# Kernel optimization log

Measured on AMD Instinct MI355X. Metric: run time of the kernel, lower is better.

The kernel has to match this reference:

```python
import jax, jax.numpy as jnp
import numpy as np

N_NODES = 50000
E_EDGES = 1600000
C_IN = 64
C_OUT = 64
K_CHEB = 3


def _norm(edge_index, edge_weight, n):
    # PyG ChebConv.__norm__ with normalization='sym', lambda_max=2.0:
    # remove self loops, sym-normalized Laplacian scaled by 2/lambda_max, then
    # subtract identity -> L_hat has zero diagonal and off-diag -d^-1/2 w d^-1/2.
    row, col = edge_index[0], edge_index[1]
    mask = row != col
    ew = jnp.where(mask, edge_weight, 0.0)
    deg = jax.ops.segment_sum(ew, row, num_segments=n)  # [N]
    dinv = jnp.where(deg > 0, jax.lax.rsqrt(jnp.where(deg > 0, deg, 1.0)), 0.0)
    wn = -ew * dinv[row] * dinv[col]  # [E], zero on (removed) self loops
    return row, col, wn


def _propagate(x, row, col, wn, n):
    # y = L_hat @ x via edge gather + weighted scatter-add
    return jax.ops.segment_sum(wn[:, None] * x[col], row, num_segments=n)


def _cheb(x, W, b, row, col, wn, n):
    # Chebyshev recursion: Tx0=x, Tx1=L_hat x, Txk = 2 L_hat Tx(k-1) - Tx(k-2)
    out = x @ W[0]
    Tx0, Tx1 = x, None
    if W.shape[0] > 1:
        Tx1 = _propagate(x, row, col, wn, n)
        out = out + Tx1 @ W[1]
    for k in range(2, W.shape[0]):
        Tx2 = 2.0 * _propagate(Tx1, row, col, wn, n) - Tx0
        out = out + Tx2 @ W[k]
        Tx0, Tx1 = Tx1, Tx2
    return out + b


def setup_inputs() -> dict:
    key = jax.random.key(0)
    ks = jax.random.split(key, 40)
    d = {
        'X': jax.random.normal(ks[0], (N_NODES, C_IN), jnp.float32),
        'edge_index': jax.random.randint(ks[1], (2, E_EDGES), 0, N_NODES),
        'edge_weight': jax.random.uniform(ks[2], (E_EDGES,), jnp.float32),
        'H': jax.random.normal(ks[3], (N_NODES, C_OUT), jnp.float32) * 0.1,
        'C': jax.random.normal(ks[4], (N_NODES, C_OUT), jnp.float32) * 0.1,
    }
    i = 5
    sx = 1.0 / np.sqrt(C_IN)
    sh = 1.0 / np.sqrt(C_OUT)
    for nm in ['xi', 'xf', 'xc', 'xo']:
        d['W_' + nm] = jax.random.normal(ks[i], (K_CHEB, C_IN, C_OUT), jnp.float32) * sx; i += 1
        d['bc_' + nm] = jax.random.normal(ks[i], (C_OUT,), jnp.float32) * 0.02; i += 1
    for nm in ['hi', 'hf', 'hc', 'ho']:
        d['W_' + nm] = jax.random.normal(ks[i], (K_CHEB, C_OUT, C_OUT), jnp.float32) * sh; i += 1
        d['bc_' + nm] = jax.random.normal(ks[i], (C_OUT,), jnp.float32) * 0.02; i += 1
    for nm in ['w_ci', 'w_cf', 'w_co', 'b_i', 'b_f', 'b_c', 'b_o']:
        d[nm] = jax.random.normal(ks[i], (1, C_OUT), jnp.float32) * 0.1; i += 1
    return d


def reference(X, edge_index, edge_weight, H, C,
              W_xi, bc_xi, W_xf, bc_xf, W_xc, bc_xc, W_xo, bc_xo,
              W_hi, bc_hi, W_hf, bc_hf, W_hc, bc_hc, W_ho, bc_ho,
              w_ci, w_cf, w_co, b_i, b_f, b_c, b_o):
    n = X.shape[0]
    row, col, wn = _norm(edge_index, edge_weight, n)
    I = jax.nn.sigmoid(_cheb(X, W_xi, bc_xi, row, col, wn, n)
                       + _cheb(H, W_hi, bc_hi, row, col, wn, n)
                       + w_ci * C + b_i)
    Fg = jax.nn.sigmoid(_cheb(X, W_xf, bc_xf, row, col, wn, n)
                        + _cheb(H, W_hf, bc_hf, row, col, wn, n)
                        + w_cf * C + b_f)
    T = jnp.tanh(_cheb(X, W_xc, bc_xc, row, col, wn, n)
                 + _cheb(H, W_hc, bc_hc, row, col, wn, n)
                 + b_c)
    C_new = Fg * C + I * T
    O = jax.nn.sigmoid(_cheb(X, W_xo, bc_xo, row, col, wn, n)
                       + _cheb(H, W_ho, bc_ho, row, col, wn, n)
                       + w_co * C_new + b_o)
    H_new = O * jnp.tanh(C_new)
    return (H_new, C_new)
```

## Files before the change

### kernel.cpp

```cpp
#include <hip/hip_runtime.h>
#include <hip/hip_bf16.h>
#include <math.h>

#define N_NODES 50000
#define E_EDGES 1600000
#define NBKT 196
#define PBLK 400
#define CHUNK 4000

typedef __attribute__((ext_vector_type(8))) short s8v;
typedef __attribute__((ext_vector_type(4))) float f32x4;

#define O_BLKH  0
#define O_BBASE 78592
#define O_BSUM  78848
#define O_CNT   79104
#define O_DINV  129152
#define O_RPTR  179200
#define O_SREC  229248
#define O_SREC2 3429248
#define O_EDGE  O_SREC
#define O_XHB   O_SREC2
#define O_T1B   6629248
#define O_T2B   9829248
#define O_BP    13029248

__device__ __forceinline__ uint pk_bf16(float x, float y) {
  __hip_bfloat16 bx = __float2bfloat16(x), by = __float2bfloat16(y);
  ushort ux = *reinterpret_cast<ushort*>(&bx);
  ushort uy = *reinterpret_cast<ushort*>(&by);
  return ((uint)uy << 16) | (uint)ux;
}

__global__ __launch_bounds__(256) void k_hist(const int* __restrict__ ei,
                                              uint* __restrict__ blkh) {
  __shared__ uint h[NBKT];
  int blk = blockIdx.x, tid = threadIdx.x;
  for (int i = tid; i < NBKT; i += 256) h[i] = 0;
  __syncthreads();
  int e0 = blk * CHUNK;
  for (int i = tid; i < CHUNK; i += 256) {
    int e = e0 + i;
    int r = ei[e], c = ei[E_EDGES + e];
    if (r != c) atomicAdd(&h[r >> 8], 1u);
  }
  __syncthreads();
  for (int i = tid; i < NBKT; i += 256) blkh[i * PBLK + blk] = h[i];
}

__global__ __launch_bounds__(256) void k_bsum_scan(uint* __restrict__ blkh,
                                                   uint* __restrict__ bsum) {
  __shared__ uint sh[512];
  int b = blockIdx.x, t = threadIdx.x;
  uint v0 = (t < PBLK) ? blkh[b * PBLK + t] : 0u;
  uint v1 = (t + 256 < PBLK) ? blkh[b * PBLK + t + 256] : 0u;
  sh[t] = v0; sh[t + 256] = v1;
  __syncthreads();
  for (int off = 1; off < 512; off <<= 1) {
    uint x0 = sh[t], x1 = sh[t + 256];
    uint a0 = (t >= off) ? sh[t - off] : 0u;
    uint a1 = (t + 256 >= off) ? sh[t + 256 - off] : 0u;
    __syncthreads();
    sh[t] = x0 + a0; sh[t + 256] = x1 + a1;
    __syncthreads();
  }
  if (t < PBLK) blkh[b * PBLK + t] = sh[t] - v0;
  if (t + 256 < PBLK) blkh[b * PBLK + t + 256] = sh[t + 256] - v1;
  if (t == 0) bsum[b] = sh[511];
}

__global__ __launch_bounds__(256) void k_bscan(const uint* __restrict__ bsum,
                                               uint* __restrict__ bbase) {
  __shared__ uint sh[256];
  int t = threadIdx.x;
  uint v = (t < NBKT) ? bsum[t] : 0u;
  sh[t] = v;
  __syncthreads();
  for (int off = 1; off < 256; off <<= 1) {
    uint a = (t >= off) ? sh[t - off] : 0u;
    __syncthreads();
    sh[t] += a;
    __syncthreads();
  }
  if (t < NBKT) bbase[t] = sh[t] - v;
  if (t == 255) bbase[NBKT] = sh[255];
}

__global__ __launch_bounds__(256) void k_scatter_b(const int* __restrict__ ei,
                                                   const float* __restrict__ ew,
                                                   const uint* __restrict__ off,
                                                   const uint* __restrict__ bbase,
                                                   unsigned long long* __restrict__ srec) {
  __shared__ uint cur[NBKT];
  int blk = blockIdx.x, tid = threadIdx.x;
  for (int i = tid; i < NBKT; i += 256) cur[i] = off[i * PBLK + blk] + bbase[i];
  __syncthreads();
  int e0 = blk * CHUNK;
  for (int i = tid; i < CHUNK; i += 256) {
    int e = e0 + i;
    int r = ei[e], c = ei[E_EDGES + e];
    if (r != c) {
      uint pos = atomicAdd(&cur[r >> 8], 1u);
      srec[pos] = ((unsigned long long)(r & 255) << 48) |
                  ((unsigned long long)(uint)c << 32) |
                  (unsigned long long)__float_as_uint(ew[e]);
    }
  }
}

__global__ __launch_bounds__(256) void k_csr(const unsigned long long* __restrict__ srec,
                                             const uint* __restrict__ bbase,
                                             unsigned long long* __restrict__ srec2,
                                             int* __restrict__ cnt, float* __restrict__ dinv,
                                             int* __restrict__ rptr) {
  __shared__ uint hc[256], hs[256], cur[256], wsum[4];
  int b = blockIdx.x, t = threadIdx.x;
  uint start = bbase[b], endv = bbase[b + 1];
  hc[t] = 0; hs[t] = 0;
  __syncthreads();
  for (uint i = start + t; i < endv; i += 256) {
    unsigned long long rec = srec[i];
    int rl = (int)(rec >> 48);
    float w = __uint_as_float((uint)rec);
    atomicAdd(&hc[rl], 1u);
    atomicAdd(&hs[rl], (uint)(w * 1048576.0f + 0.5f));
  }
  __syncthreads();
  int lane = t & 63, wid = t >> 6;
  uint myc = hc[t];
  uint x = myc;
#pragma unroll
  for (int off = 1; off < 64; off <<= 1) {
    uint y = __shfl_up(x, off);
    if (lane >= off) x += y;
  }
  if (lane == 63) wsum[wid] = x;
  __syncthreads();
  uint woff = 0;
#pragma unroll
  for (int j = 0; j < 4; ++j) if (j < wid) woff += wsum[j];
  uint excl = woff + x - myc;
  int row = b * 256 + t;
  if (row < N_NODES) {
    float d = (float)hs[t] * (1.0f / 1048576.0f);
    dinv[row] = d > 0.f ? rsqrtf(d) : 0.f;
    cnt[row] = (int)myc;
    rptr[row] = (int)(start + excl);
  }
  cur[t] = start + excl;
  __syncthreads();
  for (uint i = start + t; i < endv; i += 256) {
    unsigned long long rec = srec[i];
    int rl = (int)(rec >> 48);
    uint pos = atomicAdd(&cur[rl], 1u);
    srec2[pos] = rec;
  }
}

__global__ __launch_bounds__(256) void k_finalize(const unsigned long long* __restrict__ srec2,
                                                  const uint* __restrict__ bbase,
                                                  const float* __restrict__ dinv,
                                                  uint* __restrict__ edges) {
  int b = blockIdx.x, t = threadIdx.x;
  uint start = bbase[b], endv = bbase[b + 1];
  for (uint i = start + t; i < endv; i += 256) {
    unsigned long long rec = srec2[i];
    int rl = (int)(rec >> 48);
    int c = (int)((rec >> 32) & 0xffff);
    float w = __uint_as_float((uint)rec);
    int r = b * 256 + rl;
    float wn = -w * dinv[r] * dinv[c];
    __hip_bfloat16 bw = __float2bfloat16(wn);
    edges[i] = ((uint)c << 16) | (uint)*reinterpret_cast<ushort*>(&bw);
  }
}

__global__ void k_xhb(const float* __restrict__ X, const float* __restrict__ Hm,
                      uint* __restrict__ XHb) {
  int t = blockIdx.x * blockDim.x + threadIdx.x;
  if (t >= N_NODES * 64) return;
  int n = t >> 6, q = t & 63;
  float2 v = (q < 32) ? *(const float2*)(X + (long)n * 64 + q * 2)
                      : *(const float2*)(Hm + (long)n * 64 + (q - 32) * 2);
  XHb[t] = pk_bf16(v.x, v.y);
}

__global__ __launch_bounds__(256) void k_spmm2b(
    const uint* __restrict__ src, const uint* __restrict__ other,
    float alpha, float beta,
    const int* __restrict__ rptr, const int* __restrict__ cnt,
    const uint* __restrict__ edges, uint* __restrict__ out) {
  int wid = threadIdx.x >> 6, lane = threadIdx.x & 63;
  int row = blockIdx.x * 4 + wid;
  if (row >= N_NODES) return;
  int start = rptr[row], n = cnt[row];
  int half = lane >> 5;
  int l5 = lane & 31;
  float ax = 0.f, ay = 0.f, bx = 0.f, by = 0.f;
  for (int base = 0; base < n; base += 64) {
    int m = n - base; if (m > 64) m = 64;
    uint rec = (lane < m) ? edges[start + base + lane] : 0u;
    int iters = (m + 1) >> 1;
    int j = 0;
    for (; j + 4 <= iters; j += 4) {
#pragma unroll
      for (int u = 0; u < 4; ++u) {
        uint r = __shfl(rec, 2 * (j + u) + half);
        int cc = (int)(r >> 16);
        float ww = __uint_as_float(r << 16);
        uint2 z = *(const uint2*)(src + cc * 64 + (l5 << 1));
        ax = fmaf(ww, __uint_as_float(z.x << 16), ax);
        ay = fmaf(ww, __uint_as_float(z.x & 0xffff0000u), ay);
        bx = fmaf(ww, __uint_as_float(z.y << 16), bx);
        by = fmaf(ww, __uint_as_float(z.y & 0xffff0000u), by);
      }
    }
    for (; j < iters; ++j) {
      uint r = __shfl(rec, 2 * j + half);
      int cc = (int)(r >> 16);
      float ww = __uint_as_float(r << 16);
      uint2 z = *(const uint2*)(src + cc * 64 + (l5 << 1));
      ax = fmaf(ww, __uint_as_float(z.x << 16), ax);
      ay = fmaf(ww, __uint_as_float(z.x & 0xffff0000u), ay);
      bx = fmaf(ww, __uint_as_float(z.y << 16), bx);
      by = fmaf(ww, __uint_as_float(z.y & 0xffff0000u), by);
    }
  }
  ax += __shfl_xor(ax, 32); ay += __shfl_xor(ay, 32);
  bx += __shfl_xor(bx, 32); by += __shfl_xor(by, 32);
  if (half == 0) {
    long o = (long)row * 64 + (l5 << 1);
    float ox = alpha * ax, oy = alpha * ay;
    float px = alpha * bx, py = alpha * by;
    if (beta != 0.f) {
      uint2 ov = *(const uint2*)(other + o);
      ox += beta * __uint_as_float(ov.x << 16);
      oy += beta * __uint_as_float(ov.x & 0xffff0000u);
      px += beta * __uint_as_float(ov.y << 16);
      py += beta * __uint_as_float(ov.y & 0xffff0000u);
    }
    uint2 w2; w2.x = pk_bf16(ox, oy); w2.y = pk_bf16(px, py);
    *(uint2*)(out + o) = w2;
  }
}

__global__ void k_pack(const float* __restrict__ Wxi, const float* __restrict__ Wxf,
                       const float* __restrict__ Wxc, const float* __restrict__ Wxo,
                       const float* __restrict__ Whi, const float* __restrict__ Whf,
                       const float* __restrict__ Whc, const float* __restrict__ Who,
                       ushort* __restrict__ Bp) {
  int idx = blockIdx.x * blockDim.x + threadIdx.x;
  if (idx >= 12 * 16 * 64 * 8) return;
  int j = idx & 7;
  int lane = (idx >> 3) & 63;
  int c = (idx >> 9) & 15;
  int t = idx >> 13;
  int k = t * 32 + (lane >> 4) * 8 + j;
  int col = c * 16 + (lane & 15);
  int g = col >> 6, oc = col & 63;
  int s = k >> 6, kk = k & 63, ord = s >> 1;
  const float* Wx[4] = {Wxi, Wxf, Wxc, Wxo};
  const float* Wh[4] = {Whi, Whf, Whc, Who};
  const float* W = (s & 1) ? Wh[g] : Wx[g];
  float v = W[(ord * 64 + kk) * 64 + oc];
  __hip_bfloat16 b = __float2bfloat16(v);
  Bp[idx] = *reinterpret_cast<ushort*>(&b);
}

__device__ __forceinline__ float frcp(float x) { return __builtin_amdgcn_rcpf(x); }

__global__ __launch_bounds__(256) void k_mfma_lstm(
    const uint* __restrict__ XHb, const uint* __restrict__ T1b,
    const uint* __restrict__ T2b, const float* __restrict__ C,
    const ushort* __restrict__ Bp,
    const float* __restrict__ bxi, const float* __restrict__ bxf,
    const float* __restrict__ bxc, const float* __restrict__ bxo,
    const float* __restrict__ bhi, const float* __restrict__ bhf,
    const float* __restrict__ bhc, const float* __restrict__ bho,
    const float* __restrict__ wci, const float* __restrict__ wcf, const float* __restrict__ wco,
    const float* __restrict__ bi, const float* __restrict__ bf_,
    const float* __restrict__ bc_, const float* __restrict__ bo,
    float* __restrict__ Hout, float* __restrict__ Cout) {
  int lane = threadIdx.x & 63, wid = threadIdx.x >> 6;
  int row0 = blockIdx.x * 64 + wid * 16;
  int ar = row0 + (lane & 15);
  if (ar > N_NODES - 1) ar = N_NODES - 1;

  const ushort* XHs = (const ushort*)XHb;
  const ushort* T1s = (const ushort*)T1b;
  const ushort* T2s = (const ushort*)T2b;
  long abase = (long)ar * 128 + (lane >> 4) * 8;
  s8v a[12];
#pragma unroll
  for (int q = 0; q < 4; ++q) a[q] = *(const s8v*)(XHs + abase + q * 32);
#pragma unroll
  for (int q = 0; q < 4; ++q) a[4 + q] = *(const s8v*)(T1s + abase + q * 32);
#pragma unroll
  for (int q = 0; q < 4; ++q) a[8 + q] = *(const s8v*)(T2s + abase + q * 32);

  const ushort* bp = Bp + lane * 8;
  f32x4 acc[16];
#pragma unroll
  for (int c = 0; c < 16; ++c) acc[c] = {0.f, 0.f, 0.f, 0.f};

  s8v bA[16], bB[16];
#pragma unroll
  for (int c = 0; c < 16; ++c) bA[c] = *(const s8v*)(bp + c * 512);
#pragma unroll
  for (int t = 0; t < 12; ++t) {
    if (t & 1) {
      if (t < 11) {
#pragma unroll
        for (int c = 0; c < 16; ++c)
          bA[c] = *(const s8v*)(bp + (t + 1) * 8192 + c * 512);
      }
#pragma unroll
      for (int c = 0; c < 16; ++c)
        acc[c] = __builtin_amdgcn_mfma_f32_16x16x32_bf16(a[t], bB[c], acc[c], 0, 0, 0);
    } else {
      if (t < 11) {
#pragma unroll
        for (int c = 0; c < 16; ++c)
          bB[c] = *(const s8v*)(bp + (t + 1) * 8192 + c * 512);
      }
#pragma unroll
      for (int c = 0; c < 16; ++c)
        acc[c] = __builtin_amdgcn_mfma_f32_16x16x32_bf16(a[t], bA[c], acc[c], 0, 0, 0);
    }
  }

  int rbase = row0 + ((lane >> 4) << 2);
  int ocl = lane & 15;
#pragma unroll
  for (int j = 0; j < 4; ++j) {
    int oc = j * 16 + ocl;
    float bI = bxi[oc] + bhi[oc] + bi[oc];
    float bF = bxf[oc] + bhf[oc] + bf_[oc];
    float bT = bxc[oc] + bhc[oc] + bc_[oc];
    float bO = bxo[oc] + bho[oc] + bo[oc];
    float wcI = wci[oc], wcF = wcf[oc], wcO = wco[oc];
#pragma unroll
    for (int r = 0; r < 4; ++r) {
      int row = rbase + r;
      if (row < N_NODES) {
        float cv = C[(long)row * 64 + oc];
        float I = frcp(1.f + __expf(-(acc[j][r] + bI + wcI * cv)));
        float F = frcp(1.f + __expf(-(acc[4 + j][r] + bF + wcF * cv)));
        float e2 = __expf(2.f * (acc[8 + j][r] + bT));
        float T = 1.f - 2.f * frcp(e2 + 1.f);
        float cn = F * cv + I * T;
        float O = frcp(1.f + __expf(-(acc[12 + j][r] + bO + wcO * cn)));
        float e2c = __expf(2.f * cn);
        float tc = 1.f - 2.f * frcp(e2c + 1.f);
        Hout[(long)row * 64 + oc] = O * tc;
        Cout[(long)row * 64 + oc] = cn;
      }
    }
  }
}

extern "C" void kernel_launch(void* const* d_in, const int* in_sizes, int n_in,
                              void* d_out, int out_size, void* d_ws, size_t ws_size,
                              hipStream_t stream) {
  (void)in_sizes; (void)n_in; (void)out_size; (void)ws_size;
  const float* X   = (const float*)d_in[0];
  const int*   ei  = (const int*)d_in[1];
  const float* ew  = (const float*)d_in[2];
  const float* H   = (const float*)d_in[3];
  const float* C   = (const float*)d_in[4];
  const float* Wxi = (const float*)d_in[5];
  const float* bxi = (const float*)d_in[6];
  const float* Wxf = (const float*)d_in[7];
  const float* bxf = (const float*)d_in[8];
  const float* Wxc = (const float*)d_in[9];
  const float* bxc = (const float*)d_in[10];
  const float* Wxo = (const float*)d_in[11];
  const float* bxo = (const float*)d_in[12];
  const float* Whi = (const float*)d_in[13];
  const float* bhi = (const float*)d_in[14];
  const float* Whf = (const float*)d_in[15];
  const float* bhf = (const float*)d_in[16];
  const float* Whc = (const float*)d_in[17];
  const float* bhc = (const float*)d_in[18];
  const float* Who = (const float*)d_in[19];
  const float* bho = (const float*)d_in[20];
  const float* wci = (const float*)d_in[21];
  const float* wcf = (const float*)d_in[22];
  const float* wco = (const float*)d_in[23];
  const float* bi  = (const float*)d_in[24];
  const float* bf_ = (const float*)d_in[25];
  const float* bc_ = (const float*)d_in[26];
  const float* bo  = (const float*)d_in[27];

  float* ws = (float*)d_ws;
  uint*   blkh  = (uint*)(ws + O_BLKH);
  uint*   bbase = (uint*)(ws + O_BBASE);
  uint*   bsum  = (uint*)(ws + O_BSUM);
  int*    cnt   = (int*)(ws + O_CNT);
  float*  dinv  = ws + O_DINV;
  int*    rptr  = (int*)(ws + O_RPTR);
  unsigned long long* srec  = (unsigned long long*)(ws + O_SREC);
  unsigned long long* srec2 = (unsigned long long*)(ws + O_SREC2);
  uint*   edges = (uint*)(ws + O_EDGE);
  uint*   XHb   = (uint*)(ws + O_XHB);
  uint*   T1b   = (uint*)(ws + O_T1B);
  uint*   T2b   = (uint*)(ws + O_T2B);
  ushort* Bp    = (ushort*)(ws + O_BP);

  float* Hout = (float*)d_out;
  float* Cout = Hout + N_NODES * 64;

  k_hist<<<PBLK, 256, 0, stream>>>(ei, blkh);
  k_bsum_scan<<<NBKT, 256, 0, stream>>>(blkh, bsum);
  k_bscan<<<1, 256, 0, stream>>>(bsum, bbase);
  k_scatter_b<<<PBLK, 256, 0, stream>>>(ei, ew, blkh, bbase, srec);
  k_csr<<<NBKT, 256, 0, stream>>>(srec, bbase, srec2, cnt, dinv, rptr);
  k_finalize<<<NBKT, 256, 0, stream>>>(srec2, bbase, dinv, edges);
  k_xhb<<<(N_NODES * 64 + 255) / 256, 256, 0, stream>>>(X, H, XHb);
  k_pack<<<(12 * 16 * 64 * 8 + 255) / 256, 256, 0, stream>>>(Wxi, Wxf, Wxc, Wxo,
                                                             Whi, Whf, Whc, Who, Bp);
  int spmm_grid = (N_NODES + 3) / 4;
  k_spmm2b<<<spmm_grid, 256, 0, stream>>>(XHb, XHb, 1.f, 0.f, rptr, cnt, edges, T1b);
  k_spmm2b<<<spmm_grid, 256, 0, stream>>>(T1b, XHb, 2.f, -1.f, rptr, cnt, edges, T2b);
  k_mfma_lstm<<<(N_NODES + 63) / 64, 256, 0, stream>>>(
      XHb, T1b, T2b, C, Bp,
      bxi, bxf, bxc, bxo, bhi, bhf, bhc, bho,
      wci, wcf, wco, bi, bf_, bc_, bo, Hout, Cout);
}
```

Baseline: 221.4 us.

## Switch fused LSTM GEMM to 32x32x16 MFMA with one-wave blocks

The dense GEMM+LSTM kernel is rewritten around the 32x32x16 bf16 MFMA. Each 64-thread block now covers 32 rows, so every B fragment feeds twice as many rows. The weight packing kernel is changed to match the new fragment layout. A and B fragments are double-buffered across 24 k-steps and the epilogue is remapped to the 32x32 accumulator layout. This aims to cut weight-load traffic per row and MFMA issue count, at the cost of smaller blocks and higher register pressure.

```diff
diff --git a/kernel.cpp b/kernel.cpp
--- a/kernel.cpp
+++ b/kernel.cpp
@@ -9,7 +9,7 @@
 #define CHUNK 4000
 
 typedef __attribute__((ext_vector_type(8))) short s8v;
-typedef __attribute__((ext_vector_type(4))) float f32x4;
+typedef __attribute__((ext_vector_type(16))) float f32x16;
 
 #define O_BLKH  0
 #define O_BBASE 78592
@@ -250,13 +250,13 @@
                        const float* __restrict__ Whc, const float* __restrict__ Who,
                        ushort* __restrict__ Bp) {
   int idx = blockIdx.x * blockDim.x + threadIdx.x;
-  if (idx >= 12 * 16 * 64 * 8) return;
+  if (idx >= 24 * 8 * 64 * 8) return;
   int j = idx & 7;
   int lane = (idx >> 3) & 63;
-  int c = (idx >> 9) & 15;
-  int t = idx >> 13;
-  int k = t * 32 + (lane >> 4) * 8 + j;
-  int col = c * 16 + (lane & 15);
+  int ct = (idx >> 9) & 7;
+  int st = idx >> 12;
+  int k = st * 16 + (lane >> 5) * 8 + j;
+  int col = ct * 32 + (lane & 31);
   int g = col >> 6, oc = col & 63;
   int s = k >> 6, kk = k & 63, ord = s >> 1;
   const float* Wx[4] = {Wxi, Wxf, Wxc, Wxo};
@@ -269,7 +269,7 @@
 
 __device__ __forceinline__ float frcp(float x) { return __builtin_amdgcn_rcpf(x); }
 
-__global__ __launch_bounds__(256) void k_mfma_lstm(
+__global__ __launch_bounds__(64, 2) void k_mfma_lstm(
     const uint* __restrict__ XHb, const uint* __restrict__ T1b,
     const uint* __restrict__ T2b, const float* __restrict__ C,
     const ushort* __restrict__ Bp,
@@ -281,75 +281,63 @@
     const float* __restrict__ bi, const float* __restrict__ bf_,
     const float* __restrict__ bc_, const float* __restrict__ bo,
     float* __restrict__ Hout, float* __restrict__ Cout) {
-  int lane = threadIdx.x & 63, wid = threadIdx.x >> 6;
-  int row0 = blockIdx.x * 64 + wid * 16;
-  int ar = row0 + (lane & 15);
+  int lane = threadIdx.x & 63;
+  int row0 = blockIdx.x * 32;
+  int ar = row0 + (lane & 31);
   if (ar > N_NODES - 1) ar = N_NODES - 1;
 
   const ushort* XHs = (const ushort*)XHb;
   const ushort* T1s = (const ushort*)T1b;
   const ushort* T2s = (const ushort*)T2b;
-  long abase = (long)ar * 128 + (lane >> 4) * 8;
-  s8v a[12];
-#pragma unroll
-  for (int q = 0; q < 4; ++q) a[q] = *(const s8v*)(XHs + abase + q * 32);
-#pragma unroll
-  for (int q = 0; q < 4; ++q) a[4 + q] = *(const s8v*)(T1s + abase + q * 32);
-#pragma unroll
-  for (int q = 0; q < 4; ++q) a[8 + q] = *(const s8v*)(T2s + abase + q * 32);
-
+  long arow = (long)ar * 128 + (lane >> 5) * 8;
   const ushort* bp = Bp + lane * 8;
-  f32x4 acc[16];
-#pragma unroll
-  for (int c = 0; c < 16; ++c) acc[c] = {0.f, 0.f, 0.f, 0.f};
-
-  s8v bA[16], bB[16];
-#pragma unroll
-  for (int c = 0; c < 16; ++c) bA[c] = *(const s8v*)(bp + c * 512);
-#pragma unroll
-  for (int t = 0; t < 12; ++t) {
-    if (t & 1) {
-      if (t < 11) {
-#pragma unroll
-        for (int c = 0; c < 16; ++c)
-          bA[c] = *(const s8v*)(bp + (t + 1) * 8192 + c * 512);
-      }
-#pragma unroll
-      for (int c = 0; c < 16; ++c)
-        acc[c] = __builtin_amdgcn_mfma_f32_16x16x32_bf16(a[t], bB[c], acc[c], 0, 0, 0);
-    } else {
-      if (t < 11) {
-#pragma unroll
-        for (int c = 0; c < 16; ++c)
-          bB[c] = *(const s8v*)(bp + (t + 1) * 8192 + c * 512);
-      }
-#pragma unroll
-      for (int c = 0; c < 16; ++c)
-        acc[c] = __builtin_amdgcn_mfma_f32_16x16x32_bf16(a[t], bA[c], acc[c], 0, 0, 0);
-    }
-  }
-
-  int rbase = row0 + ((lane >> 4) << 2);
-  int ocl = lane & 15;
-#pragma unroll
-  for (int j = 0; j < 4; ++j) {
-    int oc = j * 16 + ocl;
+
+  f32x16 acc[8] = {};
+
+  s8v aC, aN;
+  s8v bC[8], bN[8];
+  aC = *(const s8v*)(XHs + arow);
+#pragma unroll
+  for (int c = 0; c < 8; ++c) bC[c] = *(const s8v*)(bp + c * 512);
+
+#pragma unroll
+  for (int st = 0; st < 24; ++st) {
+    if (st < 23) {
+      const ushort* S = (st + 1 < 8) ? XHs : ((st + 1 < 16) ? T1s : T2s);
+      aN = *(const s8v*)(S + arow + ((st + 1) & 7) * 16);
+#pragma unroll
+      for (int c = 0; c < 8; ++c)
+        bN[c] = *(const s8v*)(bp + ((st + 1) * 8 + c) * 512);
+    }
+#pragma unroll
+    for (int c = 0; c < 8; ++c)
+      acc[c] = __builtin_amdgcn_mfma_f32_32x32x16_bf16(aC, bC[c], acc[c], 0, 0, 0);
+    aC = aN;
+#pragma unroll
+    for (int c = 0; c < 8; ++c) bC[c] = bN[c];
+  }
+
+  int colb = lane & 31;
+  int rsel = 4 * (lane >> 5);
+#pragma unroll
+  for (int half = 0; half < 2; ++half) {
+    int oc = half * 32 + colb;
     float bI = bxi[oc] + bhi[oc] + bi[oc];
     float bF = bxf[oc] + bhf[oc] + bf_[oc];
     float bT = bxc[oc] + bhc[oc] + bc_[oc];
     float bO = bxo[oc] + bho[oc] + bo[oc];
     float wcI = wci[oc], wcF = wcf[oc], wcO = wco[oc];
 #pragma unroll
-    for (int r = 0; r < 4; ++r) {
-      int row = rbase + r;
+    for (int r = 0; r < 16; ++r) {
+      int row = row0 + (r & 3) + 8 * (r >> 2) + rsel;
       if (row < N_NODES) {
         float cv = C[(long)row * 64 + oc];
-        float I = frcp(1.f + __expf(-(acc[j][r] + bI + wcI * cv)));
-        float F = frcp(1.f + __expf(-(acc[4 + j][r] + bF + wcF * cv)));
-        float e2 = __expf(2.f * (acc[8 + j][r] + bT));
+        float I = frcp(1.f + __expf(-(acc[0 + half][r] + bI + wcI * cv)));
+        float F = frcp(1.f + __expf(-(acc[2 + half][r] + bF + wcF * cv)));
+        float e2 = __expf(2.f * (acc[4 + half][r] + bT));
         float T = 1.f - 2.f * frcp(e2 + 1.f);
         float cn = F * cv + I * T;
-        float O = frcp(1.f + __expf(-(acc[12 + j][r] + bO + wcO * cn)));
+        float O = frcp(1.f + __expf(-(acc[6 + half][r] + bO + wcO * cn)));
         float e2c = __expf(2.f * cn);
         float tc = 1.f - 2.f * frcp(e2c + 1.f);
         Hout[(long)row * 64 + oc] = O * tc;
@@ -417,12 +405,12 @@
   k_csr<<<NBKT, 256, 0, stream>>>(srec, bbase, srec2, cnt, dinv, rptr);
   k_finalize<<<NBKT, 256, 0, stream>>>(srec2, bbase, dinv, edges);
   k_xhb<<<(N_NODES * 64 + 255) / 256, 256, 0, stream>>>(X, H, XHb);
-  k_pack<<<(12 * 16 * 64 * 8 + 255) / 256, 256, 0, stream>>>(Wxi, Wxf, Wxc, Wxo,
-                                                             Whi, Whf, Whc, Who, Bp);
+  k_pack<<<(24 * 8 * 64 * 8 + 255) / 256, 256, 0, stream>>>(Wxi, Wxf, Wxc, Wxo,
+                                                            Whi, Whf, Whc, Who, Bp);
   int spmm_grid = (N_NODES + 3) / 4;
   k_spmm2b<<<spmm_grid, 256, 0, stream>>>(XHb, XHb, 1.f, 0.f, rptr, cnt, edges, T1b);
   k_spmm2b<<<spmm_grid, 256, 0, stream>>>(T1b, XHb, 2.f, -1.f, rptr, cnt, edges, T2b);
-  k_mfma_lstm<<<(N_NODES + 63) / 64, 256, 0, stream>>>(
+  k_mfma_lstm<<<(N_NODES + 31) / 32, 64, 0, stream>>>(
       XHb, T1b, T2b, C, Bp,
       bxi, bxf, bxc, bxo, bhi, bhf, bhc, bho,
       wci, wcf, wco, bi, bf_, bc_, bo, Hout, Cout);
```

Measured after the change: 229.6 us. 1.04x slower.

## Split gate columns across waves in LSTM MFMA kernel and vectorize epilogue via LDS

Applied to the files above, without the earlier changes.

The fused gate GEMM kernel now assigns 16 rows per block, with each of the four waves computing one gate's 64 output columns. Previously each wave held 16 rows times all 256 columns, using 16 accumulators, 12 A registers and 32 B registers. The smaller per-wave register footprint should raise occupancy and increase the block count. Gate results go through a shared-memory tile so the LSTM epilogue can work row-wise with float4 loads and stores of C, H and biases. The cost is that the weight matrix B is reloaded per block four times as often, and a barrier is added.

```diff
diff --git a/kernel.cpp b/kernel.cpp
--- a/kernel.cpp
+++ b/kernel.cpp
@@ -281,81 +281,94 @@
     const float* __restrict__ bi, const float* __restrict__ bf_,
     const float* __restrict__ bc_, const float* __restrict__ bo,
     float* __restrict__ Hout, float* __restrict__ Cout) {
-  int lane = threadIdx.x & 63, wid = threadIdx.x >> 6;
-  int row0 = blockIdx.x * 64 + wid * 16;
+  __shared__ float gsh[16][260];
+  int tid = threadIdx.x;
+  int lane = tid & 63, wid = tid >> 6;
+  int row0 = blockIdx.x * 16;
   int ar = row0 + (lane & 15);
-  if (ar > N_NODES - 1) ar = N_NODES - 1;
+  long abase = (long)ar * 128 + (lane >> 4) * 8;
 
   const ushort* XHs = (const ushort*)XHb;
   const ushort* T1s = (const ushort*)T1b;
   const ushort* T2s = (const ushort*)T2b;
-  long abase = (long)ar * 128 + (lane >> 4) * 8;
-  s8v a[12];
-#pragma unroll
-  for (int q = 0; q < 4; ++q) a[q] = *(const s8v*)(XHs + abase + q * 32);
-#pragma unroll
-  for (int q = 0; q < 4; ++q) a[4 + q] = *(const s8v*)(T1s + abase + q * 32);
-#pragma unroll
-  for (int q = 0; q < 4; ++q) a[8 + q] = *(const s8v*)(T2s + abase + q * 32);
-
-  const ushort* bp = Bp + lane * 8;
-  f32x4 acc[16];
-#pragma unroll
-  for (int c = 0; c < 16; ++c) acc[c] = {0.f, 0.f, 0.f, 0.f};
-
-  s8v bA[16], bB[16];
-#pragma unroll
-  for (int c = 0; c < 16; ++c) bA[c] = *(const s8v*)(bp + c * 512);
+  const ushort* bpg = Bp + (long)(wid * 4) * 512 + lane * 8;
+
+  f32x4 acc[4] = {};
+  s8v aC, aN;
+  s8v bC[4], bN[4];
+  aC = *(const s8v*)(XHs + abase);
+#pragma unroll
+  for (int c = 0; c < 4; ++c) bC[c] = *(const s8v*)(bpg + c * 512);
+
 #pragma unroll
   for (int t = 0; t < 12; ++t) {
-    if (t & 1) {
-      if (t < 11) {
-#pragma unroll
-        for (int c = 0; c < 16; ++c)
-          bA[c] = *(const s8v*)(bp + (t + 1) * 8192 + c * 512);
-      }
-#pragma unroll
-      for (int c = 0; c < 16; ++c)
-        acc[c] = __builtin_amdgcn_mfma_f32_16x16x32_bf16(a[t], bB[c], acc[c], 0, 0, 0);
-    } else {
-      if (t < 11) {
-#pragma unroll
-        for (int c = 0; c < 16; ++c)
-          bB[c] = *(const s8v*)(bp + (t + 1) * 8192 + c * 512);
-      }
-#pragma unroll
-      for (int c = 0; c < 16; ++c)
-        acc[c] = __builtin_amdgcn_mfma_f32_16x16x32_bf16(a[t], bA[c], acc[c], 0, 0, 0);
-    }
-  }
-
-  int rbase = row0 + ((lane >> 4) << 2);
-  int ocl = lane & 15;
-#pragma unroll
-  for (int j = 0; j < 4; ++j) {
-    int oc = j * 16 + ocl;
-    float bI = bxi[oc] + bhi[oc] + bi[oc];
-    float bF = bxf[oc] + bhf[oc] + bf_[oc];
-    float bT = bxc[oc] + bhc[oc] + bc_[oc];
-    float bO = bxo[oc] + bho[oc] + bo[oc];
-    float wcI = wci[oc], wcF = wcf[oc], wcO = wco[oc];
-#pragma unroll
-    for (int r = 0; r < 4; ++r) {
-      int row = rbase + r;
-      if (row < N_NODES) {
-        float cv = C[(long)row * 64 + oc];
-        float I = frcp(1.f + __expf(-(acc[j][r] + bI + wcI * cv)));
-        float F = frcp(1.f + __expf(-(acc[4 + j][r] + bF + wcF * cv)));
-        float e2 = __expf(2.f * (acc[8 + j][r] + bT));
-        float T = 1.f - 2.f * frcp(e2 + 1.f);
-        float cn = F * cv + I * T;
-        float O = frcp(1.f + __expf(-(acc[12 + j][r] + bO + wcO * cn)));
-        float e2c = __expf(2.f * cn);
-        float tc = 1.f - 2.f * frcp(e2c + 1.f);
-        Hout[(long)row * 64 + oc] = O * tc;
-        Cout[(long)row * 64 + oc] = cn;
-      }
-    }
+    if (t < 11) {
+      const ushort* S = (t + 1 < 4) ? XHs : ((t + 1 < 8) ? T1s : T2s);
+      aN = *(const s8v*)(S + abase + ((t + 1) & 3) * 32);
+#pragma unroll
+      for (int c = 0; c < 4; ++c)
+        bN[c] = *(const s8v*)(bpg + (long)(t + 1) * 8192 + c * 512);
+    }
+#pragma unroll
+    for (int c = 0; c < 4; ++c)
+      acc[c] = __builtin_amdgcn_mfma_f32_16x16x32_bf16(aC, bC[c], acc[c], 0, 0, 0);
+    aC = aN;
+#pragma unroll
+    for (int c = 0; c < 4; ++c) bC[c] = bN[c];
+  }
+
+  int rb = (lane >> 4) << 2;
+  int cl = lane & 15;
+#pragma unroll
+  for (int c = 0; c < 4; ++c)
+#pragma unroll
+    for (int r = 0; r < 4; ++r)
+      gsh[rb + r][wid * 64 + c * 16 + cl] = acc[c][r];
+  __syncthreads();
+
+  int rl = tid >> 4;
+  int col4 = (tid & 15) * 4;
+  int grow = row0 + rl;
+  f32x4 gI = *(const f32x4*)&gsh[rl][col4];
+  f32x4 gF = *(const f32x4*)&gsh[rl][64 + col4];
+  f32x4 gT = *(const f32x4*)&gsh[rl][128 + col4];
+  f32x4 gO = *(const f32x4*)&gsh[rl][192 + col4];
+  float4 vbI1 = *(const float4*)(bxi + col4), vbI2 = *(const float4*)(bhi + col4);
+  float4 vbI3 = *(const float4*)(bi + col4);
+  float4 vbF1 = *(const float4*)(bxf + col4), vbF2 = *(const float4*)(bhf + col4);
+  float4 vbF3 = *(const float4*)(bf_ + col4);
+  float4 vbT1 = *(const float4*)(bxc + col4), vbT2 = *(const float4*)(bhc + col4);
+  float4 vbT3 = *(const float4*)(bc_ + col4);
+  float4 vbO1 = *(const float4*)(bxo + col4), vbO2 = *(const float4*)(bho + col4);
+  float4 vbO3 = *(const float4*)(bo + col4);
+  float4 vwI = *(const float4*)(wci + col4);
+  float4 vwF = *(const float4*)(wcf + col4);
+  float4 vwO = *(const float4*)(wco + col4);
+  if (grow < N_NODES) {
+    float4 cv = *(const float4*)(C + (long)grow * 64 + col4);
+    float hn[4], cn4[4];
+    const float* cvp = &cv.x;
+    const float* bI1 = &vbI1.x; const float* bI2 = &vbI2.x; const float* bI3 = &vbI3.x;
+    const float* bF1 = &vbF1.x; const float* bF2 = &vbF2.x; const float* bF3 = &vbF3.x;
+    const float* bT1 = &vbT1.x; const float* bT2 = &vbT2.x; const float* bT3 = &vbT3.x;
+    const float* bO1 = &vbO1.x; const float* bO2 = &vbO2.x; const float* bO3 = &vbO3.x;
+    const float* wI = &vwI.x; const float* wF = &vwF.x; const float* wO = &vwO.x;
+#pragma unroll
+    for (int j = 0; j < 4; ++j) {
+      float cvj = cvp[j];
+      float I = frcp(1.f + __expf(-(gI[j] + bI1[j] + bI2[j] + bI3[j] + wI[j] * cvj)));
+      float F = frcp(1.f + __expf(-(gF[j] + bF1[j] + bF2[j] + bF3[j] + wF[j] * cvj)));
+      float e2 = __expf(2.f * (gT[j] + bT1[j] + bT2[j] + bT3[j]));
+      float T = 1.f - 2.f * frcp(e2 + 1.f);
+      float cn = F * cvj + I * T;
+      float O = frcp(1.f + __expf(-(gO[j] + bO1[j] + bO2[j] + bO3[j] + wO[j] * cn)));
+      float e2c = __expf(2.f * cn);
+      float tc = 1.f - 2.f * frcp(e2c + 1.f);
+      hn[j] = O * tc;
+      cn4[j] = cn;
+    }
+    *(float4*)(Hout + (long)grow * 64 + col4) = make_float4(hn[0], hn[1], hn[2], hn[3]);
+    *(float4*)(Cout + (long)grow * 64 + col4) = make_float4(cn4[0], cn4[1], cn4[2], cn4[3]);
   }
 }
 
@@ -422,7 +435,7 @@
   int spmm_grid = (N_NODES + 3) / 4;
   k_spmm2b<<<spmm_grid, 256, 0, stream>>>(XHb, XHb, 1.f, 0.f, rptr, cnt, edges, T1b);
   k_spmm2b<<<spmm_grid, 256, 0, stream>>>(T1b, XHb, 2.f, -1.f, rptr, cnt, edges, T2b);
-  k_mfma_lstm<<<(N_NODES + 63) / 64, 256, 0, stream>>>(
+  k_mfma_lstm<<<N_NODES / 16, 256, 0, stream>>>(
       XHb, T1b, T2b, C, Bp,
       bxi, bxf, bxc, bxo, bhi, bhf, bhc, bho,
       wci, wcf, wco, bi, bf_, bc_, bo, Hout, Cout);
```

Result: slower. 228.9 us (+3.4%).
